# Performance work log

Hardware: AMD Instinct MI355X
Metric: run time of the kernel (lower is better)

The kernel has to match this reference:

```python
import jax, jax.numpy as jnp
import numpy as np

EPS = 1e-8

def rms_norm(x, scale):
    # norm(2,-1)/sqrt(d); x / (rms + eps) * scale
    d = x.shape[-1]
    norm = jnp.sqrt(jnp.sum(x * x, axis=-1, keepdims=True))
    rms = norm / jnp.sqrt(jnp.asarray(d, x.dtype))
    return scale * (x / (rms + EPS))

def setup_inputs() -> dict:
    key = jax.random.key(0)
    B, N, C, FF = 2, 2048, 1024, 4096
    ks = jax.random.split(key, 12)
    s = 0.02
    return {
        "x":  jax.random.normal(ks[0], (B, N, C), jnp.float32),
        "wq": jax.random.normal(ks[1], (C, C), jnp.float32) * s,
        "bq": jnp.zeros((C,), jnp.float32),
        "wk": jax.random.normal(ks[2], (C, C), jnp.float32) * s,
        "bk": jnp.zeros((C,), jnp.float32),
        "wv": jax.random.normal(ks[3], (C, C), jnp.float32) * s,
        "bv": jnp.zeros((C,), jnp.float32),
        "wo": jax.random.normal(ks[4], (C, C), jnp.float32) * s,
        "bo": jnp.zeros((C,), jnp.float32),
        "scale1": jnp.ones((C,), jnp.float32),
        "scale2": jnp.ones((C,), jnp.float32),
        "w1": jax.random.normal(ks[5], (C, FF), jnp.float32) * s,
        "b1": jnp.zeros((FF,), jnp.float32),
        "w2": jax.random.normal(ks[6], (FF, C), jnp.float32) * s,
        "b2": jnp.zeros((C,), jnp.float32),
    }

def reference(x, wq, bq, wk, bk, wv, bv, wo, bo, scale1, scale2, w1, b1, w2, b2):
    B, N, C = x.shape
    H = 16
    D = C // H

    residual = x
    xn = rms_norm(x, scale1)

    def heads(y):  # [B,N,C] -> [B,H,N,D]
        return y.reshape(B, N, H, D).transpose(0, 2, 1, 3)

    q = heads(xn @ wq + bq)
    k = heads(xn @ wk + bk)
    v = heads(xn @ wv + bv)

    # apply_rotary_pos_emb with cos=sin=1: q' = q - roll(q,1,-1), same for k
    q = q - jnp.roll(q, 1, axis=-1)
    k = k - jnp.roll(k, 1, axis=-1)

    # explicit attention (no causal mask in original)
    scores = jnp.einsum('bhnd,bhmd->bhnm', q, k) / jnp.sqrt(jnp.asarray(D, x.dtype))
    probs = jax.nn.softmax(scores, axis=-1)
    attn = jnp.einsum('bhnm,bhmd->bhnd', probs, v)
    attn = attn.transpose(0, 2, 1, 3).reshape(B, N, C)
    attn = attn @ wo + bo

    x = residual + attn
    residual = x
    xn = rms_norm(x, scale2)
    h = jax.nn.gelu(xn @ w1 + b1, approximate=False)  # torch GELU default = exact
    ffn_out = h @ w2 + b2
    return residual + ffn_out
```

## Files before the change

### kernel.cpp

```cpp
#include <hip/hip_runtime.h>
#include <hip/hip_bf16.h>
#include <math.h>

typedef unsigned short u16;
typedef short s16x8 __attribute__((ext_vector_type(8)));
typedef short s16x4 __attribute__((ext_vector_type(4)));
typedef __bf16 bf16x8v __attribute__((ext_vector_type(8)));
typedef __bf16 bf16x4v __attribute__((ext_vector_type(4)));
typedef float f32x4 __attribute__((ext_vector_type(4)));
typedef unsigned short u16x4 __attribute__((ext_vector_type(4)));

struct Ptr4 { float* p[4]; };
struct TW6 {
    const float* w[6]; u16* o[6]; int mode[6];
    const float *bq, *bk, *bv; float* bqkv;
};

__device__ __forceinline__ u16 f2b(float f) {
    __hip_bfloat16 h = __float2bfloat16(f);
    return __builtin_bit_cast(u16, h);
}

__device__ __forceinline__ float exp2_fast(float x) {
#if __has_builtin(__builtin_amdgcn_exp2f)
    return __builtin_amdgcn_exp2f(x);
#else
    return exp2f(x);
#endif
}

__device__ __forceinline__ f32x4 mfma16(s16x8 a, s16x8 b, f32x4 c) {
    return __builtin_amdgcn_mfma_f32_16x16x32_bf16(
        __builtin_bit_cast(bf16x8v, a), __builtin_bit_cast(bf16x8v, b), c, 0, 0, 0);
}

__device__ __forceinline__ f32x4 mfma16k16(s16x4 a, s16x4 b, f32x4 c) {
#if __has_builtin(__builtin_amdgcn_mfma_f32_16x16x16bf16_1k)
    return __builtin_amdgcn_mfma_f32_16x16x16bf16_1k(a, b, c, 0, 0, 0);
#elif __has_builtin(__builtin_amdgcn_mfma_f32_16x16x16_bf16)
    return __builtin_amdgcn_mfma_f32_16x16x16_bf16(
        __builtin_bit_cast(bf16x4v, a), __builtin_bit_cast(bf16x4v, b), c, 0, 0, 0);
#else
    f32x4 d;
    asm volatile("v_mfma_f32_16x16x16_bf16 %0, %1, %2, %3"
                 : "=v"(d)
                 : "v"(a), "v"(b), "v"(c));
    return d;
#endif
}

__device__ __forceinline__ void gl_lds16(const void* g, void* l) {
    typedef const unsigned int __attribute__((address_space(1))) * gp_t;
    typedef unsigned int __attribute__((address_space(3))) * lp_t;
    __builtin_amdgcn_global_load_lds((gp_t)(unsigned long long)g,
                                     (lp_t)(unsigned int)(unsigned long long)l,
                                     16, 0, 0);
}

__device__ __forceinline__ float gelu_fast(float v) {
    float u = 1.5957691216f * (v + 0.044715f * v * v * v);
    return v / (1.f + __expf(-u));
}

#define QSCALE 0.1803368801111244f

__global__ __launch_bounds__(256) void prep_weights(TW6 io) {
    const int z = blockIdx.z, bx = blockIdx.x, by = blockIdx.y;
    const float* W; u16* Wt; int mode = 0, N_, K_, n0, k0;
    if (z < 4) {
        if (bx >= 32) {
            if (z == 0 && bx < 44 && by == 0) {
                const int i = (bx - 32) * 256 + threadIdx.x;
                const int d = i & 1023;
                const int dp = (d & ~63) | ((d + 63) & 63);
                float v;
                if (i < 1024) v = QSCALE * (io.bq[d] - io.bq[dp]);
                else if (i < 2048) v = io.bk[d] - io.bk[dp];
                else v = io.bv[d];
                io.bqkv[i] = v;
            }
            return;
        }
        W = io.w[z]; Wt = io.o[z]; mode = io.mode[z];
        N_ = 1024; K_ = 1024; n0 = bx * 32; k0 = by * 32;
    } else if (z == 4) {
        W = io.w[4]; Wt = io.o[4]; N_ = 4096; K_ = 1024; n0 = bx * 32; k0 = by * 32;
    } else {
        W = io.w[5]; Wt = io.o[5]; N_ = 1024; K_ = 4096; n0 = by * 32; k0 = bx * 32;
    }
    __shared__ u16 tile[32][33];
    const int tx = threadIdx.x & 31, ty = threadIdx.x >> 5;
    const int n = n0 + tx;
    const int np = (n & ~63) | ((n + 63) & 63);
    const float s = (mode == 1) ? QSCALE : 1.f;
#pragma unroll
    for (int i = 0; i < 32; i += 8) {
        const size_t r = (size_t)(k0 + ty + i) * N_;
        float v = W[r + n];
        if (mode) v = (v - W[r + np]) * s;
        tile[ty + i][tx] = f2b(v);
    }
    __syncthreads();
#pragma unroll
    for (int i = 0; i < 32; i += 8)
        Wt[(size_t)(n0 + ty + i) * K_ + k0 + tx] = tile[tx][ty + i];
}

__global__ __launch_bounds__(256) void transpose_v(const u16* __restrict__ qkv,
                                                   u16* __restrict__ vT) {
    __shared__ u16 tile[32][33];
    const int tx = threadIdx.x & 31, ty = threadIdx.x >> 5;
    const int n0 = blockIdx.x * 32, d0 = blockIdx.y * 32, bh = blockIdx.z;
    const int b = bh >> 4, h = bh & 15;
#pragma unroll
    for (int i = 0; i < 32; i += 8)
        tile[ty + i][tx] =
            qkv[(size_t)(b * 2048 + n0 + ty + i) * 3072 + 2048 + h * 64 + d0 + tx];
    __syncthreads();
#pragma unroll
    for (int i = 0; i < 32; i += 8)
        vT[((size_t)bh * 64 + d0 + ty + i) * 2048 + n0 + tx] = tile[tx][ty + i];
}

__global__ __launch_bounds__(256) void rmsnorm_kernel(const float* __restrict__ x,
                                                      const float* __restrict__ scale,
                                                      u16* __restrict__ out) {
    __shared__ float red[4];
    const int t = threadIdx.x, row = blockIdx.x;
    const float4* xr = (const float4*)(x + (size_t)row * 1024);
    float4 v = xr[t];
    float ss = v.x * v.x + v.y * v.y + v.z * v.z + v.w * v.w;
#pragma unroll
    for (int off = 1; off < 64; off <<= 1) ss += __shfl_xor(ss, off);
    if ((t & 63) == 0) red[t >> 6] = ss;
    __syncthreads();
    float tot = red[0] + red[1] + red[2] + red[3];
    float inv = 1.f / (sqrtf(tot * (1.f / 1024.f)) + 1e-8f);
    const float4* sr = (const float4*)scale;
    float4 s = sr[t];
    u16x4 o;
    o[0] = f2b(v.x * inv * s.x);
    o[1] = f2b(v.y * inv * s.y);
    o[2] = f2b(v.z * inv * s.z);
    o[3] = f2b(v.w * inv * s.w);
    ((u16x4*)(out + (size_t)row * 1024))[t] = o;
}

template <int EPI>
__global__ __launch_bounds__(256) void gemm_kernel(const u16* __restrict__ A,
                                                   const u16* __restrict__ Bt,
                                                   const float* __restrict__ bias,
                                                   const float* __restrict__ resid,
                                                   void* __restrict__ outp,
                                                   int M, int N, int K) {
    __shared__ __align__(16) u16 As[128 * 64];
    __shared__ __align__(16) u16 Bs[128 * 64];
    const int t = threadIdx.x, lane = t & 63;
    const int w = t >> 6, wm = (w >> 1) * 64, wn = (w & 1) * 64;
    const int c = lane & 15, qd = lane >> 4;
    const int n0 = blockIdx.x * 128, m0 = blockIdx.y * 128;

    const int srow = t >> 3;
    const int sch8 = ((t & 7) ^ (srow & 7)) * 8;
    const u16* Ag = A + (size_t)(m0 + srow) * K + sch8;
    const u16* Bg = Bt + (size_t)(n0 + srow) * K + sch8;
    const size_t rstride = (size_t)32 * K;

    f32x4 acc[4][4] = {};
    for (int kt = 0; kt < K; kt += 64) {
        __syncthreads();
#pragma unroll
        for (int g = 0; g < 4; g++) {
            gl_lds16(Ag + g * rstride, &As[t * 8 + g * 2048]);
            gl_lds16(Bg + g * rstride, &Bs[t * 8 + g * 2048]);
        }
        Ag += 64;
        Bg += 64;
        __syncthreads();
#pragma unroll
        for (int s = 0; s < 2; s++) {
            s16x8 a[4], b[4];
#pragma unroll
            for (int im = 0; im < 4; im++)
                a[im] = *(const s16x8*)&As[(wm + im * 16 + c) * 64 +
                                           (((s * 4 + qd) ^ (c & 7)) * 8)];
#pragma unroll
            for (int jn = 0; jn < 4; jn++)
                b[jn] = *(const s16x8*)&Bs[(wn + jn * 16 + c) * 64 +
                                           (((s * 4 + qd) ^ (c & 7)) * 8)];
#pragma unroll
            for (int im = 0; im < 4; im++)
#pragma unroll
                for (int jn = 0; jn < 4; jn++)
                    acc[im][jn] = mfma16(a[im], b[jn], acc[im][jn]);
        }
    }

#pragma unroll
    for (int im = 0; im < 4; im++) {
#pragma unroll
        for (int jn = 0; jn < 4; jn++) {
            const int colg = n0 + wn + jn * 16 + c;
            const float bv = bias[colg];
#pragma unroll
            for (int r = 0; r < 4; r++) {
                const int rowg = m0 + wm + im * 16 + qd * 4 + r;
                const size_t off = (size_t)rowg * N + colg;
                float v = acc[im][jn][r] + bv;
                if (EPI == 0) {
                    ((u16*)outp)[off] = f2b(v);
                } else if (EPI == 1) {
                    ((float*)outp)[off] = v + resid[off];
                } else {
                    ((u16*)outp)[off] = f2b(gelu_fast(v));
                }
            }
        }
    }
}

__global__ __launch_bounds__(256) void gemm_splitk(const u16* __restrict__ A,
                                                   const u16* __restrict__ Bt,
                                                   Ptr4 parts,
                                                   int N, int Ktot, int Kc) {
    __shared__ __align__(16) u16 As[128 * 64];
    __shared__ __align__(16) u16 Bs[128 * 64];
    const int t = threadIdx.x, lane = t & 63;
    const int w = t >> 6, wm = (w >> 1) * 64, wn = (w & 1) * 64;
    const int c = lane & 15, qd = lane >> 4;
    const int n0 = blockIdx.x * 128, m0 = blockIdx.y * 128;
    const int z = blockIdx.z;
    float* out = parts.p[z];

    const int srow = t >> 3;
    const int sch8 = ((t & 7) ^ (srow & 7)) * 8;
    const u16* Ag = A + (size_t)(m0 + srow) * Ktot + z * Kc + sch8;
    const u16* Bg = Bt + (size_t)(n0 + srow) * Ktot + z * Kc + sch8;
    const size_t rstride = (size_t)32 * Ktot;

    f32x4 acc[4][4] = {};
    for (int kt = 0; kt < Kc; kt += 64) {
        __syncthreads();
#pragma unroll
        for (int g = 0; g < 4; g++) {
            gl_lds16(Ag + g * rstride, &As[t * 8 + g * 2048]);
            gl_lds16(Bg + g * rstride, &Bs[t * 8 + g * 2048]);
        }
        Ag += 64;
        Bg += 64;
        __syncthreads();
#pragma unroll
        for (int s = 0; s < 2; s++) {
            s16x8 a[4], b[4];
#pragma unroll
            for (int im = 0; im < 4; im++)
                a[im] = *(const s16x8*)&As[(wm + im * 16 + c) * 64 +
                                           (((s * 4 + qd) ^ (c & 7)) * 8)];
#pragma unroll
            for (int jn = 0; jn < 4; jn++)
                b[jn] = *(const s16x8*)&Bs[(wn + jn * 16 + c) * 64 +
                                           (((s * 4 + qd) ^ (c & 7)) * 8)];
#pragma unroll
            for (int im = 0; im < 4; im++)
#pragma unroll
                for (int jn = 0; jn < 4; jn++)
                    acc[im][jn] = mfma16(a[im], b[jn], acc[im][jn]);
        }
    }

#pragma unroll
    for (int im = 0; im < 4; im++)
#pragma unroll
        for (int jn = 0; jn < 4; jn++) {
            const int colg = n0 + wn + jn * 16 + c;
#pragma unroll
            for (int r = 0; r < 4; r++) {
                const int rowg = m0 + wm + im * 16 + qd * 4 + r;
                out[(size_t)rowg * N + colg] = acc[im][jn][r];
            }
        }
}

template <int S, bool NORM>
__global__ __launch_bounds__(256) void reduce_kernel(Ptr4 parts,
                                                     const float* __restrict__ bias,
                                                     const float* __restrict__ resid,
                                                     const float* __restrict__ scale,
                                                     float* __restrict__ yout,
                                                     u16* __restrict__ xnout) {
    __shared__ float red[4];
    const int t = threadIdx.x, row = blockIdx.x;
    const size_t base = (size_t)row * 1024;
    float4 v = ((const float4*)(resid + base))[t];
    float4 bv = ((const float4*)bias)[t];
    v.x += bv.x; v.y += bv.y; v.z += bv.z; v.w += bv.w;
#pragma unroll
    for (int s = 0; s < S; s++) {
        float4 pv = ((const float4*)(parts.p[s] + base))[t];
        v.x += pv.x; v.y += pv.y; v.z += pv.z; v.w += pv.w;
    }
    ((float4*)(yout + base))[t] = v;
    if (NORM) {
        float ss = v.x * v.x + v.y * v.y + v.z * v.z + v.w * v.w;
#pragma unroll
        for (int off = 1; off < 64; off <<= 1) ss += __shfl_xor(ss, off);
        if ((t & 63) == 0) red[t >> 6] = ss;
        __syncthreads();
        float tot = red[0] + red[1] + red[2] + red[3];
        float inv = 1.f / (sqrtf(tot * (1.f / 1024.f)) + 1e-8f);
        float4 s = ((const float4*)scale)[t];
        u16x4 o;
        o[0] = f2b(v.x * inv * s.x);
        o[1] = f2b(v.y * inv * s.y);
        o[2] = f2b(v.z * inv * s.z);
        o[3] = f2b(v.w * inv * s.w);
        ((u16x4*)(xnout + base))[t] = o;
    }
}

__global__ __launch_bounds__(256, 3) void attn_kernel(const u16* __restrict__ qkv,
                                                      const u16* __restrict__ vT,
                                                      u16* __restrict__ attn) {
    __shared__ __align__(16) char smem[33792];
    __shared__ float LS[4][64];
    u16* Ks = (u16*)smem;
    u16* Vs = (u16*)(smem + 16384);

    const int t = threadIdx.x, lane = t & 63, w = t >> 6;
    const int c = lane & 15, g = lane >> 4;

    const int id = blockIdx.x;
    const int logical = (id & 7) * 128 + (id >> 3);
    const int bh = logical >> 5, qb = logical & 31;
    const int b = bh >> 4, h = bh & 15;
    const int q0 = qb * 64;
    const size_t rowbase = (size_t)b * 2048;

    const u16* kg = qkv + rowbase * 3072 + 1024 + h * 64;
    const u16* vg = vT + (size_t)bh * 64 * 2048;

    const int srow = t >> 3;
    const int sch = (t & 7) ^ (srow & 7);
    const u16* kptr = kg + (size_t)srow * 3072 + sch * 8;
    const u16* vptr = vg + (size_t)srow * 2048 + sch * 8;

    gl_lds16(kptr, &Ks[t * 8]);
    gl_lds16(kptr + (size_t)32 * 3072, &Ks[2048 + t * 8]);
    gl_lds16(vptr, &Vs[t * 8]);
    gl_lds16(vptr + (size_t)32 * 2048, &Vs[2048 + t * 8]);

    s16x8 qf[4][2];
    {
        const u16* qg = qkv + (rowbase + q0) * 3072 + h * 64;
#pragma unroll
        for (int jn = 0; jn < 4; jn++)
#pragma unroll
            for (int ks = 0; ks < 2; ks++)
                qf[jn][ks] = *(const s16x8*)&qg[(size_t)(jn * 16 + c) * 3072 +
                                                ks * 32 + g * 8];
    }
    __syncthreads();

    f32x4 acc[4][4] = {};
    float ls[4] = {};
    const int kbase = w * 16;

    for (int it = 0; it < 32; it++) {
        const int buf = it & 1;
        const u16* Kb = Ks + buf * 4096;
        const u16* Vb = Vs + buf * 4096;

        if (it + 1 < 32) {
            u16* Kn = Ks + (buf ^ 1) * 4096;
            u16* Vn = Vs + (buf ^ 1) * 4096;
            const size_t ko = (size_t)(it + 1) * 64 * 3072;
            const size_t vo = (size_t)(it + 1) * 64;
            gl_lds16(kptr + ko, &Kn[t * 8]);
            gl_lds16(kptr + ko + (size_t)32 * 3072, &Kn[2048 + t * 8]);
            gl_lds16(vptr + vo, &Vn[t * 8]);
            gl_lds16(vptr + vo + (size_t)32 * 2048, &Vn[2048 + t * 8]);
        }

        s16x8 kf[2];
#pragma unroll
        for (int ks = 0; ks < 2; ks++)
            kf[ks] = *(const s16x8*)&Kb[(kbase + c) * 64 +
                                        (((ks * 4 + g) ^ (c & 7)) * 8)];
        s16x4 vf[4];
#pragma unroll
        for (int im = 0; im < 4; im++)
            vf[im] = *(const s16x4*)&Vb[(im * 16 + c) * 64 +
                                        (((2 * w + (g >> 1)) ^ (c & 7)) * 8) +
                                        (g & 1) * 4];

        f32x4 sc[4] = {};
        __builtin_amdgcn_s_setprio(1);
#pragma unroll
        for (int ks = 0; ks < 2; ks++)
#pragma unroll
            for (int jn = 0; jn < 4; jn++)
                sc[jn] = mfma16(kf[ks], qf[jn][ks], sc[jn]);
        __builtin_amdgcn_s_setprio(0);

        s16x4 pb[4];
#pragma unroll
        for (int jn = 0; jn < 4; jn++) {
            float p0 = exp2_fast(sc[jn][0]);
            float p1 = exp2_fast(sc[jn][1]);
            float p2 = exp2_fast(sc[jn][2]);
            float p3 = exp2_fast(sc[jn][3]);
            ls[jn] += (p0 + p1) + (p2 + p3);
            pb[jn][0] = f2b(p0); pb[jn][1] = f2b(p1);
            pb[jn][2] = f2b(p2); pb[jn][3] = f2b(p3);
        }

        __builtin_amdgcn_s_setprio(1);
#pragma unroll
        for (int im = 0; im < 4; im++)
#pragma unroll
            for (int jn = 0; jn < 4; jn++)
                acc[im][jn] = mfma16k16(vf[im], pb[jn], acc[im][jn]);
        __builtin_amdgcn_s_setprio(0);
        __syncthreads();
    }

#pragma unroll
    for (int jn = 0; jn < 4; jn++) {
        float v = ls[jn];
        v += __shfl_xor(v, 16);
        v += __shfl_xor(v, 32);
        ls[jn] = v;
    }
    if (lane < 16) {
#pragma unroll
        for (int jn = 0; jn < 4; jn++) LS[w][jn * 16 + lane] = ls[jn];
    }

    float* SC = (float*)smem;
#pragma unroll
    for (int src = 3; src >= 1; --src) {
        __syncthreads();
        if (w == src) {
#pragma unroll
            for (int im = 0; im < 4; im++)
#pragma unroll
                for (int jn = 0; jn < 4; jn++)
#pragma unroll
                    for (int r = 0; r < 4; r++)
                        SC[(im * 16 + g * 4 + r) * 66 + jn * 16 + c] =
                            acc[im][jn][r];
        }
        __syncthreads();
        if (w == src - 1) {
#pragma unroll
            for (int im = 0; im < 4; im++)
#pragma unroll
                for (int jn = 0; jn < 4; jn++)
#pragma unroll
                    for (int r = 0; r < 4; r++)
                        acc[im][jn][r] +=
                            SC[(im * 16 + g * 4 + r) * 66 + jn * 16 + c];
        }
    }
    __syncthreads();

    u16* OT = (u16*)smem;
    if (w == 0) {
#pragma unroll
        for (int jn = 0; jn < 4; jn++) {
            const int q = jn * 16 + c;
            const float inv = 1.f / (LS[0][q] + LS[1][q] + LS[2][q] + LS[3][q]);
#pragma unroll
            for (int im = 0; im < 4; im++)
#pragma unroll
                for (int r = 0; r < 4; r++)
                    OT[q * 72 + im * 16 + g * 4 + r] = f2b(acc[im][jn][r] * inv);
        }
    }
    __syncthreads();

    {
        const int q = t >> 2, d0 = (t & 3) * 16;
        const int grow = b * 2048 + q0 + q;
        u16* dst = attn + (size_t)grow * 1024 + h * 64 + d0;
        *(s16x8*)dst = *(const s16x8*)&OT[q * 72 + d0];
        *((s16x8*)dst + 1) = *((const s16x8*)&OT[q * 72 + d0] + 1);
    }
}

extern "C" void kernel_launch(void* const* d_in, const int* in_sizes, int n_in,
                              void* d_out, int out_size, void* d_ws, size_t ws_size,
                              hipStream_t stream) {
    const float* x = (const float*)d_in[0];
    const float* wq = (const float*)d_in[1];
    const float* bq = (const float*)d_in[2];
    const float* wk = (const float*)d_in[3];
    const float* bk = (const float*)d_in[4];
    const float* wv = (const float*)d_in[5];
    const float* bv = (const float*)d_in[6];
    const float* wo = (const float*)d_in[7];
    const float* bo = (const float*)d_in[8];
    const float* scale1 = (const float*)d_in[9];
    const float* scale2 = (const float*)d_in[10];
    const float* w1 = (const float*)d_in[11];
    const float* b1 = (const float*)d_in[12];
    const float* w2 = (const float*)d_in[13];
    const float* b2 = (const float*)d_in[14];
    float* out = (float*)d_out;

    char* ws = (char*)d_ws;
    size_t off = 0;
    auto alloc = [&](size_t bytes) -> char* {
        char* p = ws + off;
        off += (bytes + 255) & ~(size_t)255;
        return p;
    };
    u16* wqkvT = (u16*)alloc((size_t)3072 * 1024 * 2);
    u16* woT   = (u16*)alloc((size_t)1024 * 1024 * 2);
    u16* w1T   = (u16*)alloc((size_t)4096 * 1024 * 2);
    u16* w2T   = (u16*)alloc((size_t)1024 * 4096 * 2);
    float* bqkv = (float*)alloc(3072 * 4);
    u16* xn    = (u16*)alloc((size_t)4096 * 1024 * 2);
    u16* qkv   = (u16*)alloc((size_t)4096 * 3072 * 2);
    u16* vT    = (u16*)alloc((size_t)32 * 64 * 2048 * 2);
    u16* attnb = (u16*)alloc((size_t)4096 * 1024 * 2);
    float* y1  = (float*)alloc((size_t)4096 * 1024 * 4);
    u16* hbuf  = (u16*)alloc((size_t)4096 * 4096 * 2);

    const size_t SPLIT = (size_t)4096 * 1024;
    Ptr4 po; po.p[0] = (float*)qkv; po.p[1] = (float*)qkv + SPLIT;
    po.p[2] = nullptr; po.p[3] = nullptr;
    Ptr4 pf; pf.p[0] = (float*)xn; pf.p[1] = (float*)xn + SPLIT;
    pf.p[2] = (float*)xn + 2 * SPLIT; pf.p[3] = (float*)wqkvT;

    dim3 blk(256);

    TW6 tw;
    tw.w[0] = wq; tw.o[0] = wqkvT;                          tw.mode[0] = 1;
    tw.w[1] = wk; tw.o[1] = wqkvT + (size_t)1024 * 1024;    tw.mode[1] = 2;
    tw.w[2] = wv; tw.o[2] = wqkvT + (size_t)2048 * 1024;    tw.mode[2] = 0;
    tw.w[3] = wo; tw.o[3] = woT;                            tw.mode[3] = 0;
    tw.w[4] = w1; tw.o[4] = w1T;                            tw.mode[4] = 0;
    tw.w[5] = w2; tw.o[5] = w2T;                            tw.mode[5] = 0;
    tw.bq = bq; tw.bk = bk; tw.bv = bv; tw.bqkv = bqkv;
    prep_weights<<<dim3(128, 32, 6), blk, 0, stream>>>(tw);

    rmsnorm_kernel<<<4096, blk, 0, stream>>>(x, scale1, xn);
    gemm_kernel<0><<<dim3(24, 32), blk, 0, stream>>>(xn, wqkvT, bqkv, nullptr, qkv, 4096, 3072, 1024);
    transpose_v<<<dim3(64, 2, 32), blk, 0, stream>>>(qkv, vT);
    attn_kernel<<<dim3(1024), blk, 0, stream>>>(qkv, vT, attnb);
    gemm_splitk<<<dim3(8, 32, 2), blk, 0, stream>>>(attnb, woT, po, 1024, 1024, 512);
    reduce_kernel<2, true><<<4096, blk, 0, stream>>>(po, bo, x, scale2, y1, xn);
    gemm_kernel<2><<<dim3(32, 32), blk, 0, stream>>>(xn, w1T, b1, nullptr, hbuf, 4096, 4096, 1024);
    gemm_splitk<<<dim3(8, 32, 4), blk, 0, stream>>>(hbuf, w2T, pf, 1024, 4096, 1024);
    reduce_kernel<4, false><<<4096, blk, 0, stream>>>(pf, b2, y1, nullptr, out, nullptr);
}
```

Measured before the change: 382.7 us.

## Load attention K/V fragments directly from global memory into registers, dropping LDS staging

The attention kernel no longer stages K and V tiles through double-buffered shared memory. Each wave now loads its own K and V fragments straight from global memory into registers, with K prefetched one iteration ahead using two register sets. This removes the per-iteration barrier and roughly halves the shared memory footprint. In exchange the global access patterns are less coalesced, and the V loads are not prefetched, so their latency is exposed; the kernel relies on L2 caching of the K/V blocks shared across query blocks.

```diff
diff --git a/kernel.cpp b/kernel.cpp
--- a/kernel.cpp
+++ b/kernel.cpp
@@ -321,10 +321,8 @@
 __global__ __launch_bounds__(256, 3) void attn_kernel(const u16* __restrict__ qkv,
                                                       const u16* __restrict__ vT,
                                                       u16* __restrict__ attn) {
-    __shared__ __align__(16) char smem[33792];
+    __shared__ __align__(16) char smem[16896];
     __shared__ float LS[4][64];
-    u16* Ks = (u16*)smem;
-    u16* Vs = (u16*)(smem + 16384);
 
     const int t = threadIdx.x, lane = t & 63, w = t >> 6;
     const int c = lane & 15, g = lane >> 4;
@@ -336,18 +334,8 @@
     const int q0 = qb * 64;
     const size_t rowbase = (size_t)b * 2048;
 
-    const u16* kg = qkv + rowbase * 3072 + 1024 + h * 64;
-    const u16* vg = vT + (size_t)bh * 64 * 2048;
-
-    const int srow = t >> 3;
-    const int sch = (t & 7) ^ (srow & 7);
-    const u16* kptr = kg + (size_t)srow * 3072 + sch * 8;
-    const u16* vptr = vg + (size_t)srow * 2048 + sch * 8;
-
-    gl_lds16(kptr, &Ks[t * 8]);
-    gl_lds16(kptr + (size_t)32 * 3072, &Ks[2048 + t * 8]);
-    gl_lds16(vptr, &Vs[t * 8]);
-    gl_lds16(vptr + (size_t)32 * 2048, &Vs[2048 + t * 8]);
+    const u16* kfp = qkv + (rowbase + w * 16 + c) * 3072 + 1024 + h * 64 + g * 8;
+    const u16* vfp = vT + ((size_t)bh * 64 + c) * 2048 + w * 16 + g * 4;
 
     s16x8 qf[4][2];
     {
@@ -359,49 +347,32 @@
                 qf[jn][ks] = *(const s16x8*)&qg[(size_t)(jn * 16 + c) * 3072 +
                                                 ks * 32 + g * 8];
     }
-    __syncthreads();
 
     f32x4 acc[4][4] = {};
     float ls[4] = {};
-    const int kbase = w * 16;
-
-    for (int it = 0; it < 32; it++) {
-        const int buf = it & 1;
-        const u16* Kb = Ks + buf * 4096;
-        const u16* Vb = Vs + buf * 4096;
-
-        if (it + 1 < 32) {
-            u16* Kn = Ks + (buf ^ 1) * 4096;
-            u16* Vn = Vs + (buf ^ 1) * 4096;
-            const size_t ko = (size_t)(it + 1) * 64 * 3072;
-            const size_t vo = (size_t)(it + 1) * 64;
-            gl_lds16(kptr + ko, &Kn[t * 8]);
-            gl_lds16(kptr + ko + (size_t)32 * 3072, &Kn[2048 + t * 8]);
-            gl_lds16(vptr + vo, &Vn[t * 8]);
-            gl_lds16(vptr + vo + (size_t)32 * 2048, &Vn[2048 + t * 8]);
-        }
-
-        s16x8 kf[2];
-#pragma unroll
-        for (int ks = 0; ks < 2; ks++)
-            kf[ks] = *(const s16x8*)&Kb[(kbase + c) * 64 +
-                                        (((ks * 4 + g) ^ (c & 7)) * 8)];
-        s16x4 vf[4];
+
+    s16x8 kfA[2], kfB[2];
+    s16x4 vf[4];
+
+    auto loadK = [&](s16x8 (&dst)[2], int it) {
+        const u16* p = kfp + (size_t)it * 64 * 3072;
+        dst[0] = *(const s16x8*)p;
+        dst[1] = *(const s16x8*)(p + 32);
+    };
+    auto loadV = [&](int it) {
 #pragma unroll
         for (int im = 0; im < 4; im++)
-            vf[im] = *(const s16x4*)&Vb[(im * 16 + c) * 64 +
-                                        (((2 * w + (g >> 1)) ^ (c & 7)) * 8) +
-                                        (g & 1) * 4];
-
+            vf[im] = *(const s16x4*)(vfp + (size_t)(im * 16) * 2048 + it * 64);
+    };
+    auto compute = [&](s16x8 (&kf_)[2]) {
         f32x4 sc[4] = {};
         __builtin_amdgcn_s_setprio(1);
 #pragma unroll
         for (int ks = 0; ks < 2; ks++)
 #pragma unroll
             for (int jn = 0; jn < 4; jn++)
-                sc[jn] = mfma16(kf[ks], qf[jn][ks], sc[jn]);
+                sc[jn] = mfma16(kf_[ks], qf[jn][ks], sc[jn]);
         __builtin_amdgcn_s_setprio(0);
-
         s16x4 pb[4];
 #pragma unroll
         for (int jn = 0; jn < 4; jn++) {
@@ -413,7 +384,6 @@
             pb[jn][0] = f2b(p0); pb[jn][1] = f2b(p1);
             pb[jn][2] = f2b(p2); pb[jn][3] = f2b(p3);
         }
-
         __builtin_amdgcn_s_setprio(1);
 #pragma unroll
         for (int im = 0; im < 4; im++)
@@ -421,7 +391,17 @@
             for (int jn = 0; jn < 4; jn++)
                 acc[im][jn] = mfma16k16(vf[im], pb[jn], acc[im][jn]);
         __builtin_amdgcn_s_setprio(0);
-        __syncthreads();
+    };
+
+    loadK(kfA, 0);
+    for (int t2 = 0; t2 < 16; ++t2) {
+        const int it0 = t2 * 2;
+        loadK(kfB, it0 + 1);
+        loadV(it0);
+        compute(kfA);
+        if (t2 < 15) loadK(kfA, it0 + 2);
+        loadV(it0 + 1);
+        compute(kfB);
     }
 
 #pragma unroll
```

Measured after the change: 425.1 us. 1.11x slower.

## Triple-buffer K/V tiles in attention with manual vmcnt waits

Applied to the files above, without the earlier changes.

Replaces the double-buffered K/V LDS staging in the attention kernel with a three-stage ring. Tiles are now prefetched two iterations ahead, and a partial s_waitcnt vmcnt(4) plus a single barrier per iteration stands in for the trailing __syncthreads. This is meant to hide more global-load latency behind the MFMA work. In exchange LDS use per block grows from about 33KB to 48KB, which may limit how many blocks fit on a CU under the 3-blocks launch bound. It also relies on hand-counted outstanding-load numbers being correct.

```diff
diff --git a/kernel.cpp b/kernel.cpp
--- a/kernel.cpp
+++ b/kernel.cpp
@@ -321,10 +321,9 @@
 __global__ __launch_bounds__(256, 3) void attn_kernel(const u16* __restrict__ qkv,
                                                       const u16* __restrict__ vT,
                                                       u16* __restrict__ attn) {
-    __shared__ __align__(16) char smem[33792];
+    __shared__ __align__(16) char smem[49152];
     __shared__ float LS[4][64];
-    u16* Ks = (u16*)smem;
-    u16* Vs = (u16*)(smem + 16384);
+    u16* SM = (u16*)smem;
 
     const int t = threadIdx.x, lane = t & 63, w = t >> 6;
     const int c = lane & 15, g = lane >> 4;
@@ -344,10 +343,15 @@
     const u16* kptr = kg + (size_t)srow * 3072 + sch * 8;
     const u16* vptr = vg + (size_t)srow * 2048 + sch * 8;
 
-    gl_lds16(kptr, &Ks[t * 8]);
-    gl_lds16(kptr + (size_t)32 * 3072, &Ks[2048 + t * 8]);
-    gl_lds16(vptr, &Vs[t * 8]);
-    gl_lds16(vptr + (size_t)32 * 2048, &Vs[2048 + t * 8]);
+    auto stage = [&](int it, int bi) {
+        u16* B = SM + bi * 8192;
+        const size_t ko = (size_t)it * 64 * 3072;
+        const size_t vo = (size_t)it * 64;
+        gl_lds16(kptr + ko, &B[t * 8]);
+        gl_lds16(kptr + ko + (size_t)32 * 3072, &B[2048 + t * 8]);
+        gl_lds16(vptr + vo, &B[4096 + t * 8]);
+        gl_lds16(vptr + vo + (size_t)32 * 2048, &B[6144 + t * 8]);
+    };
 
     s16x8 qf[4][2];
     {
@@ -359,27 +363,27 @@
                 qf[jn][ks] = *(const s16x8*)&qg[(size_t)(jn * 16 + c) * 3072 +
                                                 ks * 32 + g * 8];
     }
-    __syncthreads();
+
+    stage(0, 0);
+    stage(1, 1);
 
     f32x4 acc[4][4] = {};
     float ls[4] = {};
     const int kbase = w * 16;
 
+    int cur = 0, nxt2 = 2;
     for (int it = 0; it < 32; it++) {
-        const int buf = it & 1;
-        const u16* Kb = Ks + buf * 4096;
-        const u16* Vb = Vs + buf * 4096;
-
-        if (it + 1 < 32) {
-            u16* Kn = Ks + (buf ^ 1) * 4096;
-            u16* Vn = Vs + (buf ^ 1) * 4096;
-            const size_t ko = (size_t)(it + 1) * 64 * 3072;
-            const size_t vo = (size_t)(it + 1) * 64;
-            gl_lds16(kptr + ko, &Kn[t * 8]);
-            gl_lds16(kptr + ko + (size_t)32 * 3072, &Kn[2048 + t * 8]);
-            gl_lds16(vptr + vo, &Vn[t * 8]);
-            gl_lds16(vptr + vo + (size_t)32 * 2048, &Vn[2048 + t * 8]);
-        }
+        if (it < 31)
+            asm volatile("s_waitcnt vmcnt(4) lgkmcnt(0)" ::: "memory");
+        else
+            asm volatile("s_waitcnt vmcnt(0) lgkmcnt(0)" ::: "memory");
+        __builtin_amdgcn_s_barrier();
+        __builtin_amdgcn_sched_barrier(0);
+
+        if (it + 2 < 32) stage(it + 2, nxt2);
+
+        const u16* Kb = SM + cur * 8192;
+        const u16* Vb = Kb + 4096;
 
         s16x8 kf[2];
 #pragma unroll
@@ -421,7 +425,9 @@
             for (int jn = 0; jn < 4; jn++)
                 acc[im][jn] = mfma16k16(vf[im], pb[jn], acc[im][jn]);
         __builtin_amdgcn_s_setprio(0);
-        __syncthreads();
+
+        cur = (cur == 2) ? 0 : cur + 1;
+        nxt2 = (nxt2 == 2) ? 0 : nxt2 + 1;
     }
 
 #pragma unroll
```

After: 373.6 us. 1.02x faster.
